# Kernel tuning notes

Measured on AMD Instinct MI355X. Metric: run time of the kernel, lower is better.

The kernel has to match this reference:

```python
import jax, jax.numpy as jnp
import numpy as np

# Geometry (scaled-up version of the ODL setup in the source):
# angles: uniform partition of [0, pi) with A cells -> centers (j+0.5)*pi/A
# detector: uniform partition of [-2, 2] with D cells
# volume: uniform_discr([-1,-1],[1,1],(N,N)), axis 0 = x, axis 1 = y
A, D, N = 400, 512, 256
KS = 11  # fbp_ker_size
DPHI = np.pi / A      # angle cell width (adjoint weighting)
S_MIN, DS = -2.0, 4.0 / D


def _det_coords():
    """Fractional detector index u[a, i, j] for every (angle, pixel)."""
    phis = (jnp.arange(A, dtype=jnp.float32) + 0.5) * jnp.float32(np.pi / A)
    xs = jnp.float32(-1.0) + (jnp.arange(N, dtype=jnp.float32) + 0.5) * jnp.float32(2.0 / N)
    X, Y = jnp.meshgrid(xs, xs, indexing='ij')              # [N,N]
    sin_p = jnp.sin(phis)[:, None, None]
    cos_p = jnp.cos(phis)[:, None, None]
    # ODL parallel-beam: detector axis (-sin phi, cos phi)
    S = -X[None] * sin_p + Y[None] * cos_p                  # [A,N,N]
    return (S - S_MIN) / DS - 0.5                           # fractional index


def backproject(sino):
    """Parallel-beam adjoint (backprojection). sino: [C,A,D] -> [C,N,N].
    Linear interpolation along detector, zero outside, angle-weighted sum.
    Scan over angles keeps the working set at O(C*N*N)."""
    U = _det_coords()                         # [A,N,N]
    sino_a = jnp.transpose(sino, (1, 0, 2))   # [A,C,D]
    C = sino.shape[0]

    def body(acc, inputs):
        u, g = inputs                         # u: [N,N], g: [C,D]
        k0 = jnp.floor(u).astype(jnp.int32)
        w = u - k0.astype(u.dtype)
        k0c = jnp.clip(k0, 0, D - 1)
        k1c = jnp.clip(k0 + 1, 0, D - 1)
        m0 = ((k0 >= 0) & (k0 < D)).astype(g.dtype)
        m1 = ((k0 + 1 >= 0) & (k0 + 1 < D)).astype(g.dtype)
        val = g[:, k0c] * ((1.0 - w) * m0)[None] + g[:, k1c] * (w * m1)[None]
        return acc + val, None

    acc0 = jnp.zeros((C, N, N), sino.dtype)
    acc, _ = jax.lax.scan(body, acc0, (U, sino_a))
    return acc * jnp.float32(DPHI)


def conv2d(x, w, b, pad):
    y = jax.lax.conv_general_dilated(
        x, w, window_strides=(1, 1), padding=pad,
        dimension_numbers=('NCHW', 'OIHW', 'NCHW'))
    return y + b[None, :, None, None]


def setup_inputs() -> dict:
    key = jax.random.key(0)
    ks = jax.random.split(key, 7)
    x = jax.random.normal(ks[0], (1, 1, A, D), jnp.float32)
    w_det = jax.random.normal(ks[1], (32, 1, 1, KS), jnp.float32) * 0.3
    b_det = jax.random.normal(ks[2], (32,), jnp.float32) * 0.1
    w1 = jax.random.normal(ks[3], (32, 32, 3, 3), jnp.float32) * 0.06
    b1 = jax.random.normal(ks[4], (32,), jnp.float32) * 0.1
    w2 = jax.random.normal(ks[5], (1, 32, 3, 3), jnp.float32) * 0.06
    b2 = jax.random.normal(ks[6], (32,), jnp.float32)[:32][:1].repeat(32)[:32] * 0.0 + jax.random.normal(ks[6], (32,), jnp.float32)[:1].repeat(32) * 0.1
    b2 = jax.random.normal(ks[6], (1,), jnp.float32) * 0.1
    return {"x": x, "w_det": w_det, "b_det": b_det, "w1": w1, "b1": b1,
            "w2": w2, "b2": b2}


def reference(x, w_det, b_det, w1, b1, w2, b2):
    # detector conv: pad both sides by KS-1, slice off right -> causal padding
    y = conv2d(x, w_det, b_det, ((0, 0), (KS - 1, KS - 1)))[..., :-(KS - 1)]  # [1,32,A,D]
    vol = backproject(y[0])[None]                                             # [1,32,N,N]
    y = conv2d(vol, w1, b1, ((2, 2), (2, 2)))[..., :-2, :-2]
    y = jax.nn.sigmoid(y)
    y = conv2d(y, w2, b2, ((2, 2), (2, 2)))[..., :-2, :-2]
    return jax.nn.sigmoid(y)
```

## Files before the change

kernel.cpp:

```cpp
#include <hip/hip_runtime.h>
#include <hip/hip_fp16.h>
#include <math.h>
#include <stdint.h>

#define A_ANG 400
#define DDET  512
#define NVOL  256
#define CCH   32
#define KSZ   11
#define PI_F  3.14159265358979323846f

#define NCHUNK 5
#define APC (A_ANG / NCHUNK)
#define RING 6
#define PD   4

typedef _Float16 half8 __attribute__((ext_vector_type(8)));
typedef __fp16  fp16x2 __attribute__((ext_vector_type(2)));
typedef float   floatx4 __attribute__((ext_vector_type(4)));

typedef __attribute__((address_space(3))) uint32_t       lds_u32;
typedef const __attribute__((address_space(1))) uint32_t glb_u32;
#define GLL4(gp, lp) \
  __builtin_amdgcn_global_load_lds((glb_u32*)(gp), (lds_u32*)(lp), 4, 0, 0)

__global__ __launch_bounds__(256) void k_detconv(const float* __restrict__ x,
                                                 const float* __restrict__ wdet,
                                                 const float* __restrict__ bdet,
                                                 __half* __restrict__ y2h,
                                                 float* __restrict__ vol) {
  __shared__ float wl[CCH * KSZ];
  __shared__ float bl[CCH];
  int t = threadIdx.x;
  for (int e = t; e < CCH * KSZ; e += 256) wl[e] = wdet[e];
  if (t < CCH) bl[t] = bdet[t];
  __syncthreads();

  int idx = blockIdx.x * 256 + t;
  if (idx < NVOL * NVOL * CCH) vol[idx] = 0.0f;
  int d2 = idx & 255;
  int c = (idx >> 8) & 31;
  int a = idx >> 13;
  const float* xr = x + a * DDET;
  int d0 = 2 * d2;
  float acc0 = bl[c], acc1 = bl[c];
#pragma unroll
  for (int k = 0; k < KSZ; ++k) {
    float wv = wl[c * KSZ + k];
    int dd0 = d0 + k - (KSZ - 1);
    int dd1 = dd0 + 1;
    float xv0 = (dd0 >= 0) ? xr[dd0] : 0.0f;
    float xv1 = (dd1 >= 0) ? xr[dd1] : 0.0f;
    acc0 = fmaf(wv, xv0, acc0);
    acc1 = fmaf(wv, xv1, acc1);
  }
  __half2 hv = __floats2half2_rn(acc0, acc1);
  *reinterpret_cast<__half2*>(y2h + ((size_t)(a * CCH + c) * DDET + d0)) = hv;
}

__global__ __launch_bounds__(256, 4) void k_backproj(const __half* __restrict__ y2h,
                                                     float* __restrict__ vol) {
  __shared__ __align__(16) uint32_t s_ring[RING * 1024];
  __shared__ float s_sin[APC];
  __shared__ float s_cos[APC];

  int t = threadIdx.x;
  int lane = t & 63;
  int w = t >> 6;
  int h = lane >> 4;
  int r = lane & 15;

  int tile = blockIdx.x & 255;
  int chunk = blockIdx.x >> 8;
  int a0 = chunk * APC;

  for (int a = t; a < APC; a += 256) {
    float ph = ((float)(a0 + a) + 0.5f) * (PI_F / (float)A_ANG);
    float sv, cv;
    sincosf(ph, &sv, &cv);
    s_sin[a] = sv;
    s_cos[a] = cv;
  }

  int bi = tile >> 4, bj = tile & 15;
  int wi = w >> 1, wj = w & 1;
  int hh = h & 1;
  int ga = h >> 1;
  float Xcw = 124.0f - (float)(bi * 16 + 8 * wi);
  float Ycw = (float)(bj * 16 + 8 * wj) - 124.0f;
  float Xlh = 127.5f - (float)(bi * 16 + 8 * wi + 4 * hh + (r >> 3));
  float Yl  = (float)(bj * 16 + 8 * wj + (r & 7)) - 127.5f;

  int bpaA = (((h & 2) | 0) * 16 + r) << 2;
  int bpaB = (((h & 2) | 1) * 16 + r) << 2;

  int goffv[4];
#pragma unroll
  for (int i2 = 0; i2 < 4; ++i2)
    goffv[i2] = ((lane >> 3) << 8) + (lane & 7) + i2 * 2048;
  int rdoff0 = r * 8 + hh * 4;
  int rdoff1 = (16 + r) * 8 + hh * 4;

  const uint32_t* y2a = (const uint32_t*)y2h + (size_t)a0 * 8192;

  floatx4 acc[4][2];
#pragma unroll
  for (int m = 0; m < 4; ++m)
#pragma unroll
    for (int n = 0; n < 2; ++n) acc[m][n] = (floatx4){0.f, 0.f, 0.f, 0.f};

  __syncthreads();

  auto issue = [&](int an, int slot) {
    float sp = s_sin[an], cp = s_cos[an];
    float ucw = fmaf(Xcw, sp, fmaf(Ycw, cp, 255.5f));
    int ibw = ((int)floorf(ucw) - 7) & ~1;
    int wb = __builtin_amdgcn_readfirstlane(an * 8192 + (ibw >> 1));
    const uint32_t* src = y2a + wb;
    uint32_t* lb = s_ring + slot * 1024 + w * 256;
#pragma unroll
    for (int i2 = 0; i2 < 4; ++i2) GLL4(src + goffv[i2], lb + i2 * 64);
  };

  auto computePair = [&](int k, int sl0, int sl1) {
    int ak = k + ga;
    int sa = ga ? sl1 : sl0;
    float sp = s_sin[ak], cp = s_cos[ak];
    float ucw = fmaf(Xcw, sp, fmaf(Ycw, cp, 255.5f));
    int ibw = ((int)floorf(ucw) - 7) & ~1;
    const uint32_t* rbw = s_ring + sa * 1024 + w * 256;
    half8 bf0 = *(const half8*)(rbw + rdoff0);
    half8 bf1 = *(const half8*)(rbw + rdoff1);
    uint32_t lov[2], msgv[2];
    float us = fmaf(Xlh, sp, fmaf(Yl, cp, 255.5f));
#pragma unroll
    for (int cch = 0; cch < 2; ++cch) {
      float fl = floorf(us);
      float wf = us - fl;
      int e = (int)fl - ibw;
      float w0 = 1.0f - wf;
      union { fp16x2 hv; uint32_t u; } p01;
      p01.hv = __builtin_amdgcn_cvt_pkrtz(w0, wf);
      uint64_t v64 = ((uint64_t)p01.u) << ((e & 1) << 4);
      lov[cch] = (uint32_t)v64;
      msgv[cch] = (uint32_t)(v64 >> 32) | ((uint32_t)(e >> 1) << 16);
      us = fmaf(-2.0f, sp, us);
    }
    __builtin_amdgcn_s_setprio(1);
#pragma unroll
    for (int m = 0; m < 4; ++m) {
      int bpa = (m < 2) ? bpaA : bpaB;
      uint32_t lom =
          (uint32_t)__builtin_amdgcn_ds_bpermute(bpa, (int)((m & 1) ? lov[1] : lov[0]));
      uint32_t mm =
          (uint32_t)__builtin_amdgcn_ds_bpermute(bpa, (int)((m & 1) ? msgv[1] : msgv[0]));
      int qm = (int)(mm >> 16) - 4 * hh;
      uint32_t him = mm & 0xFFFFu;
      union { uint32_t u[4]; half8 v; } af;
#pragma unroll
      for (int j2 = 0; j2 < 4; ++j2) {
        uint32_t rj = (qm == j2) ? lom : 0u;
        rj = (qm == j2 - 1) ? him : rj;
        af.u[j2] = rj;
      }
      acc[m][0] =
          __builtin_amdgcn_mfma_f32_16x16x32_f16(af.v, bf0, acc[m][0], 0, 0, 0);
      acc[m][1] =
          __builtin_amdgcn_mfma_f32_16x16x32_f16(af.v, bf1, acc[m][1], 0, 0, 0);
    }
    __builtin_amdgcn_s_setprio(0);
  };

#pragma unroll
  for (int p = 0; p < PD; ++p) issue(p, p);
  asm volatile("s_waitcnt vmcnt(8)" ::: "memory");

  int sk = 0;
  for (int k = 0; k < APC; k += 2) {
    int s1 = sk + 1; if (s1 >= RING) s1 -= RING;
    computePair(k, sk, s1);
    int s4 = sk + 4; if (s4 >= RING) s4 -= RING;
    int s5 = s4 + 1; if (s5 >= RING) s5 -= RING;
    int a4 = k + 4; a4 = (a4 < APC) ? a4 : (APC - 1);
    int a5 = k + 5; a5 = (a5 < APC) ? a5 : (APC - 1);
    issue(a4, s4);
    issue(a5, s5);
    asm volatile("s_waitcnt vmcnt(8)" ::: "memory");
    sk += 2; if (sk >= RING) sk -= RING;
  }

  asm volatile("s_waitcnt vmcnt(0)" ::: "memory");
  __syncthreads();

  float* s_epi = (float*)s_ring;
  const float DPHI = PI_F / (float)A_ANG;
  size_t gbase = ((size_t)(bi * 16) * NVOL + (size_t)(bj * 16)) * CCH;
#pragma unroll
  for (int n = 0; n < 2; ++n) {
    if (n) __syncthreads();
#pragma unroll
    for (int m = 0; m < 4; ++m)
#pragma unroll
      for (int jr = 0; jr < 4; ++jr) {
        int p = 4 * h + jr;
        int px = (8 * wi + 2 * m + (p >> 3)) * 16 + 8 * wj + (p & 7);
        s_epi[r * 257 + px] = acc[m][n][jr] * DPHI;
      }
    __syncthreads();
#pragma unroll
    for (int mm = 0; mm < 16; ++mm) {
      int f = mm * 256 + t;
      int c16 = f & 15;
      int p2 = f >> 4;
      int jj = p2 & 15, ii = p2 >> 4;
      float v = s_epi[c16 * 257 + p2];
      atomicAdd(vol + gbase + ((size_t)ii * NVOL + jj) * CCH + 16 * n + c16, v);
    }
  }
}

__global__ __launch_bounds__(256) void k_conv1(const float* __restrict__ vol,
                                               const float* __restrict__ w1,
                                               const float* __restrict__ b1,
                                               float* __restrict__ out1) {
  __shared__ uint32_t wlds[9 * 2 * 256];
  int t = threadIdx.x;
  for (int u = t; u < 9 * 2 * 256; u += 256) {
    int q = u & 3;
    int lane_s = (u >> 2) & 63;
    int blk = u >> 8;
    int p = blk >> 1, n = blk & 1;
    int hs = lane_s >> 4, rs = lane_s & 15;
    int oc = 16 * n + rs;
    int ci0 = 8 * hs + 2 * q;
    int di = p / 3, dj = p % 3;
    float a0 = w1[((oc * CCH + ci0) * 3 + di) * 3 + dj];
    float a1 = w1[((oc * CCH + ci0 + 1) * 3 + di) * 3 + dj];
    union { fp16x2 hv; uint32_t u32; } pk;
    pk.hv = __builtin_amdgcn_cvt_pkrtz(a0, a1);
    wlds[u] = pk.u32;
  }
  __syncthreads();

  int lane = t & 63;
  int w = t >> 6;
  int h = lane >> 4, r = lane & 15;
  int px0 = (blockIdx.x * 4 + w) * 16;
  int i = px0 >> 8, j0 = px0 & 255;

  floatx4 acc[2];
  float bv0 = b1[r], bv1 = b1[16 + r];
  acc[0] = (floatx4){bv0, bv0, bv0, bv0};
  acc[1] = (floatx4){bv1, bv1, bv1, bv1};

#pragma unroll
  for (int p = 0; p < 9; ++p) {
    int di = p / 3, dj = p % 3;
    int ii = i + di - 2;
    if (ii >= 0) {
      int jrp = j0 + r + dj - 2;
      int jc = max(jrp, 0);
      const float4* ap =
          (const float4*)(vol + ((size_t)(ii * NVOL + jc)) * CCH + 8 * h);
      float4 v0 = ap[0], v1 = ap[1];
      if (jrp < 0) {
        v0 = (float4){0.f, 0.f, 0.f, 0.f};
        v1 = (float4){0.f, 0.f, 0.f, 0.f};
      }
      union { uint32_t u[4]; half8 v; } af;
      union { fp16x2 hv; uint32_t u32; } c0, c1, c2, c3;
      c0.hv = __builtin_amdgcn_cvt_pkrtz(v0.x, v0.y);
      c1.hv = __builtin_amdgcn_cvt_pkrtz(v0.z, v0.w);
      c2.hv = __builtin_amdgcn_cvt_pkrtz(v1.x, v1.y);
      c3.hv = __builtin_amdgcn_cvt_pkrtz(v1.z, v1.w);
      af.u[0] = c0.u32; af.u[1] = c1.u32; af.u[2] = c2.u32; af.u[3] = c3.u32;
      half8 bf0 = *(const half8*)(wlds + (p * 2 + 0) * 256 + lane * 4);
      half8 bf1 = *(const half8*)(wlds + (p * 2 + 1) * 256 + lane * 4);
      acc[0] = __builtin_amdgcn_mfma_f32_16x16x32_f16(af.v, bf0, acc[0], 0, 0, 0);
      acc[1] = __builtin_amdgcn_mfma_f32_16x16x32_f16(af.v, bf1, acc[1], 0, 0, 0);
    }
  }

#pragma unroll
  for (int n = 0; n < 2; ++n)
#pragma unroll
    for (int jr = 0; jr < 4; ++jr) {
      float s = 1.0f / (1.0f + expf(-acc[n][jr]));
      out1[(size_t)(px0 + 4 * h + jr) * CCH + 16 * n + r] = s;
    }
}

__global__ __launch_bounds__(256) void k_conv2(const float* __restrict__ s1,
                                               const float* __restrict__ w2,
                                               const float* __restrict__ b2,
                                               float* __restrict__ out) {
  __shared__ float wl[9 * CCH];
  __shared__ float red[256];
  int t = threadIdx.x;
  for (int e = t; e < 9 * CCH; e += 256) {
    int ci = e & 31, p = e >> 5;
    int di = p / 3, dj = p % 3;
    wl[e] = w2[ci * 9 + di * 3 + dj];
  }
  __syncthreads();

  int px0 = blockIdx.x * 64;
  int pix = px0 + (t >> 2);
  int j = pix & 255, i = pix >> 8;
  int cg = (t & 3) * 8;

  float acc = 0.0f;
#pragma unroll
  for (int p = 0; p < 9; ++p) {
    int di = p / 3, dj = p % 3;
    int ii = i + di - 2, jj = j + dj - 2;
    if (ii >= 0 && jj >= 0) {
      const float4* ip4 =
          (const float4*)(s1 + ((size_t)(ii * NVOL + jj)) * CCH + cg);
      const float4* wv4 = (const float4*)(&wl[p * CCH + cg]);
      float4 v0 = ip4[0], v1 = ip4[1];
      float4 w0 = wv4[0], w1 = wv4[1];
      acc = fmaf(v0.x, w0.x, acc);
      acc = fmaf(v0.y, w0.y, acc);
      acc = fmaf(v0.z, w0.z, acc);
      acc = fmaf(v0.w, w0.w, acc);
      acc = fmaf(v1.x, w1.x, acc);
      acc = fmaf(v1.y, w1.y, acc);
      acc = fmaf(v1.z, w1.z, acc);
      acc = fmaf(v1.w, w1.w, acc);
    }
  }
  red[t] = acc;
  __syncthreads();
  if (t < 64) {
    float4 rv = *(const float4*)(&red[4 * t]);
    float s = rv.x + rv.y + rv.z + rv.w + b2[0];
    out[px0 + t] = 1.0f / (1.0f + expf(-s));
  }
}

extern "C" void kernel_launch(void* const* d_in, const int* in_sizes, int n_in,
                              void* d_out, int out_size, void* d_ws,
                              size_t ws_size, hipStream_t stream) {
  const float* x    = (const float*)d_in[0];
  const float* wdet = (const float*)d_in[1];
  const float* bdet = (const float*)d_in[2];
  const float* w1   = (const float*)d_in[3];
  const float* b1   = (const float*)d_in[4];
  const float* w2   = (const float*)d_in[5];
  const float* b2   = (const float*)d_in[6];
  float* out = (float*)d_out;

  float* ws = (float*)d_ws;
  __half* y2h = (__half*)ws;
  float* vol  = ws + (A_ANG * CCH * DDET) / 2;
  float* sig1 = vol + NVOL * NVOL * CCH;

  k_detconv<<<dim3((A_ANG * CCH * DDET / 2) / 256), dim3(256), 0, stream>>>(
      x, wdet, bdet, y2h, vol);
  k_backproj<<<dim3(256 * NCHUNK), dim3(256), 0, stream>>>(y2h, vol);
  k_conv1<<<dim3(256 * 4), dim3(256), 0, stream>>>(vol, w1, b1, sig1);
  k_conv2<<<dim3(256 * 4), dim3(256), 0, stream>>>(sig1, w2, b2, out);
}
```

Baseline: 147.9 us.

## Load backprojection B fragments directly from global into registers with double buffering

Replaces the LDS ring buffer filled by global_load_lds with direct per-lane 16-byte global loads of the half-precision sinogram fragments into registers, software-pipelined two angle pairs ahead. This removes the LDS staging traffic, the ring-slot bookkeeping and the manual vmcnt waits, and shrinks shared memory to the epilogue buffer, which may allow more resident blocks. In exchange each lane issues unaligned vector global loads that depend on L1/L2 locality, and latency hiding now relies on the compiler's waitcnt placement with only one pair of lookahead.

Measured after the change: 145.0 us (median of 2 runs). Within noise of the previous version (-2.0%).

```diff
diff --git a/kernel.cpp b/kernel.cpp
--- a/kernel.cpp
+++ b/kernel.cpp
@@ -12,17 +12,11 @@
 
 #define NCHUNK 5
 #define APC (A_ANG / NCHUNK)
-#define RING 6
-#define PD   4
 
 typedef _Float16 half8 __attribute__((ext_vector_type(8)));
 typedef __fp16  fp16x2 __attribute__((ext_vector_type(2)));
 typedef float   floatx4 __attribute__((ext_vector_type(4)));
-
-typedef __attribute__((address_space(3))) uint32_t       lds_u32;
-typedef const __attribute__((address_space(1))) uint32_t glb_u32;
-#define GLL4(gp, lp) \
-  __builtin_amdgcn_global_load_lds((glb_u32*)(gp), (lds_u32*)(lp), 4, 0, 0)
+typedef uint32_t u32x4a __attribute__((ext_vector_type(4), aligned(4)));
 
 __global__ __launch_bounds__(256) void k_detconv(const float* __restrict__ x,
                                                  const float* __restrict__ wdet,
@@ -60,7 +54,7 @@
 
 __global__ __launch_bounds__(256, 4) void k_backproj(const __half* __restrict__ y2h,
                                                      float* __restrict__ vol) {
-  __shared__ __align__(16) uint32_t s_ring[RING * 1024];
+  __shared__ float s_epi[16 * 257];
   __shared__ float s_sin[APC];
   __shared__ float s_cos[APC];
 
@@ -94,14 +88,8 @@
   int bpaA = (((h & 2) | 0) * 16 + r) << 2;
   int bpaB = (((h & 2) | 1) * 16 + r) << 2;
 
-  int goffv[4];
-#pragma unroll
-  for (int i2 = 0; i2 < 4; ++i2)
-    goffv[i2] = ((lane >> 3) << 8) + (lane & 7) + i2 * 2048;
-  int rdoff0 = r * 8 + hh * 4;
-  int rdoff1 = (16 + r) * 8 + hh * 4;
-
   const uint32_t* y2a = (const uint32_t*)y2h + (size_t)a0 * 8192;
+  int choff = r * 256 + 4 * hh;
 
   floatx4 acc[4][2];
 #pragma unroll
@@ -111,26 +99,24 @@
 
   __syncthreads();
 
-  auto issue = [&](int an, int slot) {
-    float sp = s_sin[an], cp = s_cos[an];
-    float ucw = fmaf(Xcw, sp, fmaf(Ycw, cp, 255.5f));
-    int ibw = ((int)floorf(ucw) - 7) & ~1;
-    int wb = __builtin_amdgcn_readfirstlane(an * 8192 + (ibw >> 1));
-    const uint32_t* src = y2a + wb;
-    uint32_t* lb = s_ring + slot * 1024 + w * 256;
-#pragma unroll
-    for (int i2 = 0; i2 < 4; ++i2) GLL4(src + goffv[i2], lb + i2 * 64);
-  };
-
-  auto computePair = [&](int k, int sl0, int sl1) {
+  union bfrag { u32x4a u4; half8 v; };
+
+  auto loadPair = [&](int k, bfrag& b0, bfrag& b1) {
     int ak = k + ga;
-    int sa = ga ? sl1 : sl0;
+    ak = (ak < APC) ? ak : (APC - 1);
     float sp = s_sin[ak], cp = s_cos[ak];
     float ucw = fmaf(Xcw, sp, fmaf(Ycw, cp, 255.5f));
     int ibw = ((int)floorf(ucw) - 7) & ~1;
-    const uint32_t* rbw = s_ring + sa * 1024 + w * 256;
-    half8 bf0 = *(const half8*)(rbw + rdoff0);
-    half8 bf1 = *(const half8*)(rbw + rdoff1);
+    const uint32_t* p = y2a + ak * 8192 + choff + (ibw >> 1);
+    b0.u4 = *(const u32x4a*)p;
+    b1.u4 = *(const u32x4a*)(p + 4096);
+  };
+
+  auto computePair = [&](int k, bfrag b0, bfrag b1) {
+    int ak = k + ga;
+    float sp = s_sin[ak], cp = s_cos[ak];
+    float ucw = fmaf(Xcw, sp, fmaf(Ycw, cp, 255.5f));
+    int ibw = ((int)floorf(ucw) - 7) & ~1;
     uint32_t lov[2], msgv[2];
     float us = fmaf(Xlh, sp, fmaf(Yl, cp, 255.5f));
 #pragma unroll
@@ -164,35 +150,25 @@
         af.u[j2] = rj;
       }
       acc[m][0] =
-          __builtin_amdgcn_mfma_f32_16x16x32_f16(af.v, bf0, acc[m][0], 0, 0, 0);
+          __builtin_amdgcn_mfma_f32_16x16x32_f16(af.v, b0.v, acc[m][0], 0, 0, 0);
       acc[m][1] =
-          __builtin_amdgcn_mfma_f32_16x16x32_f16(af.v, bf1, acc[m][1], 0, 0, 0);
+          __builtin_amdgcn_mfma_f32_16x16x32_f16(af.v, b1.v, acc[m][1], 0, 0, 0);
     }
     __builtin_amdgcn_s_setprio(0);
   };
 
-#pragma unroll
-  for (int p = 0; p < PD; ++p) issue(p, p);
-  asm volatile("s_waitcnt vmcnt(8)" ::: "memory");
-
-  int sk = 0;
-  for (int k = 0; k < APC; k += 2) {
-    int s1 = sk + 1; if (s1 >= RING) s1 -= RING;
-    computePair(k, sk, s1);
-    int s4 = sk + 4; if (s4 >= RING) s4 -= RING;
-    int s5 = s4 + 1; if (s5 >= RING) s5 -= RING;
-    int a4 = k + 4; a4 = (a4 < APC) ? a4 : (APC - 1);
-    int a5 = k + 5; a5 = (a5 < APC) ? a5 : (APC - 1);
-    issue(a4, s4);
-    issue(a5, s5);
-    asm volatile("s_waitcnt vmcnt(8)" ::: "memory");
-    sk += 2; if (sk >= RING) sk -= RING;
-  }
-
-  asm volatile("s_waitcnt vmcnt(0)" ::: "memory");
-  __syncthreads();
-
-  float* s_epi = (float*)s_ring;
+  bfrag A0, A1, B0, B1;
+  loadPair(0, A0, A1);
+  loadPair(2, B0, B1);
+  for (int k = 0; k < APC; k += 4) {
+    computePair(k, A0, A1);
+    loadPair(k + 4, A0, A1);
+    computePair(k + 2, B0, B1);
+    loadPair(k + 6, B0, B1);
+  }
+
+  __syncthreads();
+
   const float DPHI = PI_F / (float)A_ANG;
   size_t gbase = ((size_t)(bi * 16) * NVOL + (size_t)(bj * 16)) * CCH;
 #pragma unroll
```
